# Optimization experiments

Measured on AMD Instinct MI355X. Metric: run time of the kernel, lower is better.

The kernel has to match this reference:

```python
import jax, jax.numpy as jnp
import numpy as np

B, S, D = 2, 1024, 1024
E, DG, L, H = 8, 256, 3, 2048
THR = 0.3


def setup_inputs() -> dict:
    key = jax.random.key(0)
    ks = jax.random.split(key, 10)
    hidden_states = jax.random.normal(ks[0], (B, S, D), jnp.float32)
    X = jax.random.normal(ks[1], (E, D), jnp.float32) * 0.02          # gate expert embeddings
    W_mlp = jax.random.normal(ks[2], (D, DG), jnp.float32) * (D ** -0.5)
    W_struct = jax.random.normal(ks[3], (D, DG), jnp.float32) * (D ** -0.5)
    conv_W = jax.random.normal(ks[4], (L, DG, DG), jnp.float32) * (DG ** -0.5)
    w_proj = jax.random.normal(ks[5], (DG,), jnp.float32) * (DG ** -0.5)
    W1 = jax.random.normal(ks[6], (E, D, H), jnp.float32) * (D ** -0.5)  # per-expert FFN up
    W2 = jax.random.normal(ks[7], (E, H, D), jnp.float32) * (H ** -0.5)  # per-expert FFN down
    lamb = jnp.asarray(1.5, jnp.float32)
    theta = jnp.asarray([E / 2.0], jnp.float32)
    count = jnp.zeros((E,), jnp.float32)
    # --- structural graph, precomputed once as in GoEgate.get_edges ---
    expn = np.asarray(jax.nn.silu(X @ W_struct))
    expn = expn / np.linalg.norm(expn, axis=1, keepdims=True)
    sim = expn @ expn.T
    y, perc, mask = 1.0, 0.0, None
    while perc < THR:
        mask = np.abs(sim) >= y
        perc = mask.sum() / (E * E)
        y -= 0.01
    N = E + 1  # experts + 1 token node per block
    A = np.zeros((N, N), np.float32)
    A[:E, :E] = mask
    A[:E, E] = 1.0
    A[E, :E] = 1.0
    A = A + np.eye(N, dtype=np.float32)  # GCNConv adds self-loops (experts end at 2, token node at 1)
    dinv = 1.0 / np.sqrt(A.sum(1))
    A_hat = jnp.asarray(dinv[:, None] * A * dinv[None, :])  # D^-1/2 (A+I) D^-1/2, [N, N]
    return dict(hidden_states=hidden_states, X=X, W_mlp=W_mlp, W_struct=W_struct,
                conv_W=conv_W, w_proj=w_proj, W1=W1, W2=W2, lamb=lamb, theta=theta,
                count=count, A_hat=A_hat, top_k=2)


def reference(hidden_states, X, W_mlp, W_struct, conv_W, w_proj, W1, W2,
              lamb, theta, count, A_hat, top_k):
    act = jax.nn.silu
    b, s, d = hidden_states.shape
    x2d = hidden_states.reshape(-1, d)            # [T, D]
    T = x2d.shape[0]
    # ---- GoEgate ----
    xg = act(x2d @ W_mlp)                          # [T, DG]
    expg = act(X @ W_struct)                       # [E, DG]
    node_x = jnp.concatenate(
        [jnp.broadcast_to(expg[None], (T, E, DG)), xg[:, None, :]], axis=1)  # [T, N, DG]
    for l in range(conv_W.shape[0]):
        node_x = act(jnp.einsum('nm,tmg->tng', A_hat, node_x @ conv_W[l]))   # GCN layer
    logits = (node_x @ w_proj)[:, :E]              # drop token-node column -> [T, E]
    probs = jax.nn.softmax(logits, axis=-1)        # router_logits after softmax
    rw, sel = jax.lax.top_k(probs, top_k)          # [T, k]
    # count accumulation (uses un-normalized topk weights)
    cmat = jnp.zeros((T, E), probs.dtype).at[jnp.arange(T)[:, None], sel].add(rw)
    now_count = count + cmat.sum(0) * top_k        # [E]
    rw = rw / rw.sum(-1, keepdims=True)            # normalize routing weights
    w_full = jnp.zeros((T, E), probs.dtype).at[jnp.arange(T)[:, None], sel].add(rw)
    # ---- per-expert FFN dispatch/combine (dense reference) ----
    h = act(jnp.einsum('td,edh->eth', x2d, W1))    # [E, T, H]
    expert_out = jnp.einsum('eth,ehd->etd', h, W2) # [E, T, D]
    final = jnp.einsum('etd,te->td', expert_out, w_full).reshape(b, s, d)
    loss_component = jnp.concatenate(
        [probs, now_count[None, :], jnp.broadcast_to(lamb, (1, E)),
         jnp.broadcast_to(theta, (1, E))], axis=0)  # [T+3, E]
    return final, loss_component
```

## Files before the change

### kernel.cpp

```cpp
#include <hip/hip_runtime.h>
#include <math.h>

#define TT 2048
#define Dm 1024
#define DGc 256
#define Ec 8
#define Nc 9
#define Hc 2048
#define PADMAX 5120
#define NT64MAX 80

typedef __attribute__((ext_vector_type(8))) short short8v;
typedef __attribute__((ext_vector_type(4))) float f32x4;

typedef __attribute__((address_space(1))) const void gvoid;
typedef __attribute__((address_space(3))) void svoid;

__device__ __forceinline__ void gll16(const void* g, void* l) {
    __builtin_amdgcn_global_load_lds((gvoid*)g, (svoid*)l, 16, 0, 0);
}

__device__ __forceinline__ float silu_f(float x) { return x / (1.f + __expf(-x)); }

__device__ __forceinline__ unsigned short bf16_rne(float f) {
    union { float f; unsigned u; } u; u.f = f;
    return (unsigned short)((u.u + 0x7fffu + ((u.u >> 16) & 1u)) >> 16);
}
__device__ __forceinline__ float bf16_to_f(unsigned short h) {
    union { unsigned u; float f; } u; u.u = ((unsigned)h) << 16; return u.f;
}
__device__ __forceinline__ void split2(float x, unsigned short& h, unsigned short& l) {
    h = bf16_rne(x);
    l = bf16_rne(x - bf16_to_f(h));
}

__device__ __forceinline__ void tsplit_body(const float* S, unsigned short* dh,
        unsigned short* dl, int R, int C, int r0, int c0, int tid, float (*t)[36]) {
    int i = tid >> 3, j4 = (tid & 7) * 4;
    *(float4*)&t[i][j4] = *(const float4*)&S[(size_t)(r0 + i) * C + c0 + j4];
    __syncthreads();
    int ci = tid >> 3, r4 = (tid & 7) * 4;
    ushort4 h, l;
    split2(t[r4 + 0][ci], h.x, l.x);
    split2(t[r4 + 1][ci], h.y, l.y);
    split2(t[r4 + 2][ci], h.z, l.z);
    split2(t[r4 + 3][ci], h.w, l.w);
    size_t o = (size_t)(c0 + ci) * R + r0 + r4;
    *(ushort4*)&dh[o] = h;
    *(ushort4*)&dl[o] = l;
}

__device__ __forceinline__ void tc64_body(const float* S, unsigned short* D,
        int R, int C, int r0, int c0, int tid, float* sb) {
    int r = tid >> 2;
    int cb = (tid & 3) * 16;
    const float* src = &S[(size_t)(r0 + r) * C + c0 + cb];
    int rot = 4 * (r & 15);
#pragma unroll
    for (int q = 0; q < 4; q++) {
        float4 v = *(const float4*)&src[q * 4];
        int cc = (cb + q * 4 + rot) & 63;
        *(float4*)&sb[r * 68 + cc] = v;
    }
    __syncthreads();
    int ci = tid >> 2;
    int rseg = (tid & 3) * 16;
    short8v o0, o1;
#pragma unroll
    for (int k = 0; k < 8; k++) {
        int r2 = rseg + k;
        int cc = (ci + 4 * (r2 & 15)) & 63;
        o0[k] = (short)bf16_rne(sb[r2 * 68 + cc]);
    }
#pragma unroll
    for (int k = 8; k < 16; k++) {
        int r2 = rseg + k;
        int cc = (ci + 4 * (r2 & 15)) & 63;
        o1[k - 8] = (short)bf16_rne(sb[r2 * 68 + cc]);
    }
    unsigned short* dst = &D[(size_t)(c0 + ci) * R + r0 + rseg];
    *(short8v*)&dst[0] = o0;
    *(short8v*)&dst[8] = o1;
}

__global__ __launch_bounds__(256) void k_tcslab(const float* src, unsigned short* dst,
                                                int R, int C) {
    __shared__ float sb[64 * 68];
    int per = (R / 64) * (C / 64);
    int e = blockIdx.x / per;
    int rem = blockIdx.x % per;
    int cpr = C / 64;
    int r0 = (rem / cpr) * 64;
    int c0 = (rem % cpr) * 64;
    tc64_body(src + (size_t)e * R * C, dst + (size_t)e * R * C, R, C, r0, c0,
              threadIdx.x, sb);
}

__global__ __launch_bounds__(256) void k_prep(const float* hs, const float* Wmlp,
        const float* convW, const float* X, const float* Wst,
        const float* count, const float* lamb, const float* theta,
        unsigned short* hs_hi, unsigned short* hs_lo,
        unsigned short* WmT_h, unsigned short* WmT_l,
        unsigned short* WcT_h, unsigned short* WcT_l,
        float* Xpart, float* out, int* tcnt,
        const float* W1, const float* W2,
        unsigned short* W1T, unsigned short* W2T) {
    __shared__ float sbuf[64 * 68];
    int b = blockIdx.x;
    int tid = threadIdx.x;
    if (b < 1024) {
        size_t i = ((size_t)b * 256 + tid) * 8;
        float4 v0 = *(const float4*)&hs[i];
        float4 v1 = *(const float4*)&hs[i + 4];
        ushort4 h0, l0, h1, l1;
        split2(v0.x, h0.x, l0.x); split2(v0.y, h0.y, l0.y);
        split2(v0.z, h0.z, l0.z); split2(v0.w, h0.w, l0.w);
        split2(v1.x, h1.x, l1.x); split2(v1.y, h1.y, l1.y);
        split2(v1.z, h1.z, l1.z); split2(v1.w, h1.w, l1.w);
        *(ushort4*)&hs_hi[i] = h0; *(ushort4*)&hs_hi[i + 4] = h1;
        *(ushort4*)&hs_lo[i] = l0; *(ushort4*)&hs_lo[i + 4] = l1;
    } else if (b < 1280) {
        int i2 = b - 1024;
        tsplit_body(Wmlp, WmT_h, WmT_l, Dm, DGc, (i2 >> 3) * 32, (i2 & 7) * 32,
                    tid, (float(*)[36])sbuf);
    } else if (b < 1472) {
        int i2 = b - 1280;
        int e = i2 >> 6, rem = i2 & 63;
        tsplit_body(convW + (size_t)e * DGc * DGc, WcT_h + (size_t)e * DGc * DGc,
                    WcT_l + (size_t)e * DGc * DGc, DGc, DGc,
                    (rem >> 3) * 32, (rem & 7) * 32, tid, (float(*)[36])sbuf);
    } else if (b < 1488) {
        float (*xs)[64] = (float(*)[64])sbuf;
        int p = b - 1472;
        int kb = p * 64;
        if (tid < 128) {
            int e = tid >> 4, k4 = (tid & 15) * 4;
            *(float4*)&xs[e][k4] = *(const float4*)&X[(size_t)e * Dm + kb + k4];
        }
        __syncthreads();
        float acc[Ec];
#pragma unroll
        for (int e = 0; e < Ec; e++) acc[e] = 0.f;
#pragma unroll 4
        for (int k = 0; k < 64; k++) {
            float w = Wst[(size_t)(kb + k) * DGc + tid];
#pragma unroll
            for (int e = 0; e < Ec; e++) acc[e] += xs[e][k] * w;
        }
#pragma unroll
        for (int e = 0; e < Ec; e++) Xpart[(size_t)p * Ec * DGc + e * DGc + tid] = acc[e];
    } else if (b == 1488) {
        if (tid < Ec) {
            float* loss = out + (size_t)TT * Dm;
            loss[(size_t)(TT + 1) * Ec + tid] = lamb[0];
            loss[(size_t)(TT + 2) * Ec + tid] = theta[0];
        }
        for (int i = tid; i < TT; i += 256) tcnt[i] = 0;
    } else {
        int i = b - 1489;
        if (i < 4096) {
            int e = i >> 9, rem = i & 511;
            int r0 = (rem >> 5) * 64, c0 = (rem & 31) * 64;
            tc64_body(W1 + (size_t)e * Dm * Hc, W1T + (size_t)e * Dm * Hc,
                      Dm, Hc, r0, c0, tid, sbuf);
        } else {
            i -= 4096;
            int e = i >> 9, rem = i & 511;
            int r0 = (rem >> 4) * 64, c0 = (rem & 15) * 64;
            tc64_body(W2 + (size_t)e * Hc * Dm, W2T + (size_t)e * Hc * Dm,
                      Hc, Dm, r0, c0, tid, sbuf);
        }
    }
}

__global__ __launch_bounds__(256) void k_gA(const float* Xpart, const float* W0,
                                            float* Gpart) {
    int g = threadIdx.x;
    int kb = blockIdx.x * 32;
    __shared__ float xs[Ec][32];
    {
        int m = g >> 5, k = g & 31;
        float s = 0.f;
#pragma unroll
        for (int p = 0; p < 16; p++)
            s += Xpart[(size_t)p * Ec * DGc + m * DGc + kb + k];
        xs[m][k] = silu_f(s);
    }
    __syncthreads();
    float acc[Ec];
#pragma unroll
    for (int e = 0; e < Ec; e++) acc[e] = 0.f;
#pragma unroll 4
    for (int k = 0; k < 32; k++) {
        float w = W0[(size_t)(kb + k) * DGc + g];
#pragma unroll
        for (int e = 0; e < Ec; e++) acc[e] += xs[e][k] * w;
    }
#pragma unroll
    for (int e = 0; e < Ec; e++)
        Gpart[(size_t)blockIdx.x * Ec * DGc + e * DGc + g] = acc[e];
}

__global__ __launch_bounds__(256) void k_s1fin(const float* Gpart, const float* Ahat,
                                               float* S1) {
    int g = threadIdx.x;
    float Gl[Ec];
#pragma unroll
    for (int m = 0; m < Ec; m++) {
        float s = 0.f;
#pragma unroll
        for (int kb = 0; kb < 8; kb++)
            s += Gpart[(size_t)kb * Ec * DGc + m * DGc + g];
        Gl[m] = s;
    }
#pragma unroll
    for (int n = 0; n < Nc; n++) {
        float s = 0.f;
#pragma unroll
        for (int m = 0; m < Ec; m++) s += Ahat[n * Nc + m] * Gl[m];
        S1[n * DGc + g] = s;
    }
}

template<int BM, int KD, int KS, int BK, int EPI>
__global__ __launch_bounds__(256) void gemm4s(const unsigned short* Ah,
        const unsigned short* Al, const unsigned short* Bh, const unsigned short* Bl,
        float* Cf, unsigned short* Oh, unsigned short* Ol) {
    constexpr int FM = BM / 32;
    constexpr int KLEN = KD / KS;
    constexpr int CH = BK / 8;
    constexpr int RPP = 256 / CH;
    constexpr int APASS = BM / RPP;
    constexpr int BPASS = 128 / RPP;
    constexpr int KKS = BK / 32;
    int m0 = blockIdx.x * BM, n0 = blockIdx.y * 128;
    int k0 = blockIdx.z * KLEN;
    __shared__ __align__(16) unsigned short AsH[BM * BK];
    __shared__ __align__(16) unsigned short AsL[BM * BK];
    __shared__ __align__(16) unsigned short BsH[128 * BK];
    __shared__ __align__(16) unsigned short BsL[128 * BK];
    int tid = threadIdx.x, lane = tid & 63, wid = tid >> 6;
    int wr = wid >> 1, wc = wid & 1, lo = lane & 15, hi = lane >> 4;

    f32x4 acc[FM][4];
#pragma unroll
    for (int m = 0; m < FM; m++)
#pragma unroll
        for (int n = 0; n < 4; n++) acc[m][n] = (f32x4)(0.f);

    int arow = tid / CH;
    int cswz = ((tid & (CH - 1)) ^ (arow & (CH - 1))) * 8;
    const unsigned short* AgH = Ah + (size_t)(m0 + arow) * KD + cswz;
    const unsigned short* AgL = Al + (size_t)(m0 + arow) * KD + cswz;
    const unsigned short* BgH = Bh + (size_t)(n0 + arow) * KD + cswz;
    const unsigned short* BgL = Bl + (size_t)(n0 + arow) * KD + cswz;

    for (int kb = k0; kb < k0 + KLEN; kb += BK) {
#pragma unroll
        for (int r = 0; r < APASS; r++) {
            gll16(AgH + (size_t)r * RPP * KD + kb, (char*)AsH + r * 4096 + tid * 16);
            gll16(AgL + (size_t)r * RPP * KD + kb, (char*)AsL + r * 4096 + tid * 16);
        }
#pragma unroll
        for (int r = 0; r < BPASS; r++) {
            gll16(BgH + (size_t)r * RPP * KD + kb, (char*)BsH + r * 4096 + tid * 16);
            gll16(BgL + (size_t)r * RPP * KD + kb, (char*)BsL + r * 4096 + tid * 16);
        }
        __syncthreads();
#pragma unroll
        for (int kk = 0; kk < KKS; kk++) {
            int csel = ((kk * 4 + hi) ^ (lo & (CH - 1))) * 8;
            short8v ah[FM], al[FM], bh[4], bl[4];
#pragma unroll
            for (int m = 0; m < FM; m++) {
                ah[m] = *(const short8v*)&AsH[(wr * (BM / 2) + m * 16 + lo) * BK + csel];
                al[m] = *(const short8v*)&AsL[(wr * (BM / 2) + m * 16 + lo) * BK + csel];
            }
#pragma unroll
            for (int n = 0; n < 4; n++) {
                bh[n] = *(const short8v*)&BsH[(wc * 64 + n * 16 + lo) * BK + csel];
                bl[n] = *(const short8v*)&BsL[(wc * 64 + n * 16 + lo) * BK + csel];
            }
#pragma unroll
            for (int m = 0; m < FM; m++)
#pragma unroll
                for (int n = 0; n < 4; n++)
                    acc[m][n] = __builtin_amdgcn_mfma_f32_16x16x32_bf16(ah[m], bh[n], acc[m][n], 0, 0, 0);
#pragma unroll
            for (int m = 0; m < FM; m++)
#pragma unroll
                for (int n = 0; n < 4; n++)
                    acc[m][n] = __builtin_amdgcn_mfma_f32_16x16x32_bf16(ah[m], bl[n], acc[m][n], 0, 0, 0);
#pragma unroll
            for (int m = 0; m < FM; m++)
#pragma unroll
                for (int n = 0; n < 4; n++)
                    acc[m][n] = __builtin_amdgcn_mfma_f32_16x16x32_bf16(al[m], bh[n], acc[m][n], 0, 0, 0);
        }
        __syncthreads();
    }

#pragma unroll
    for (int m = 0; m < FM; m++) {
#pragma unroll
        for (int n = 0; n < 4; n++) {
            int col = n0 + wc * 64 + n * 16 + lo;
#pragma unroll
            for (int r = 0; r < 4; r++) {
                int row = m0 + wr * (BM / 2) + m * 16 + hi * 4 + r;
                if (EPI == 0) {
                    Cf[(size_t)row * 256 + col] = acc[m][n][r];
                } else if (EPI == 3) {
                    Cf[((size_t)blockIdx.z * TT + row) * 256 + col] = acc[m][n][r];
                } else {
                    float s = silu_f(acc[m][n][r]);
                    unsigned short h, l;
                    split2(s, h, l);
                    Oh[(size_t)row * 256 + col] = h;
                    Ol[(size_t)row * 256 + col] = l;
                }
            }
        }
    }
}

__global__ __launch_bounds__(256) void k_finsplit(const float* src,
        unsigned short* dh, unsigned short* dl) {
    size_t i = ((size_t)blockIdx.x * 256 + threadIdx.x) * 4;
    float4 v0 = *(const float4*)&src[i];
    float4 v1 = *(const float4*)&src[(size_t)TT * DGc + i];
    float4 v2 = *(const float4*)&src[(size_t)2 * TT * DGc + i];
    float4 v3 = *(const float4*)&src[(size_t)3 * TT * DGc + i];
    float4 v = make_float4(v0.x + v1.x + v2.x + v3.x, v0.y + v1.y + v2.y + v3.y,
                           v0.z + v1.z + v2.z + v3.z, v0.w + v1.w + v2.w + v3.w);
    ushort4 h, l;
    split2(silu_f(v.x), h.x, l.x);
    split2(silu_f(v.y), h.y, l.y);
    split2(silu_f(v.z), h.z, l.z);
    split2(silu_f(v.w), h.w, l.w);
    *(ushort4*)&dh[i] = h;
    *(ushort4*)&dl[i] = l;
}

__global__ __launch_bounds__(256) void k_l1(const float* ypart, const float* S1,
        const float* Ahat, unsigned short* nh, unsigned short* nl) {
    int t = blockIdx.x, g = threadIdx.x;
    float yv = ypart[(size_t)t * DGc + g] + ypart[(size_t)TT * DGc + (size_t)t * DGc + g];
#pragma unroll
    for (int n = 0; n < Nc; n++) {
        float c = Ahat[n * Nc + Ec];
        float s = silu_f(S1[n * DGc + g] + c * yv);
        unsigned short h, l;
        split2(s, h, l);
        size_t o = ((size_t)t * Nc + n) * DGc + g;
        nh[o] = h; nl[o] = l;
    }
}

__global__ __launch_bounds__(256) void k_mix2(const float* Z, const float* Ahat,
        unsigned short* nh, unsigned short* nl) {
    int t = blockIdx.x, g = threadIdx.x;
    __shared__ float A[Nc * Nc];
    if (g < Nc * Nc) A[g] = Ahat[g];
    __syncthreads();
    float z[Nc];
#pragma unroll
    for (int m = 0; m < Nc; m++) z[m] = Z[((size_t)t * Nc + m) * DGc + g];
#pragma unroll
    for (int n = 0; n < Nc; n++) {
        float s = 0.f;
#pragma unroll
        for (int m = 0; m < Nc; m++) s += A[n * Nc + m] * z[m];
        s = silu_f(s);
        unsigned short h, l;
        split2(s, h, l);
        size_t o = ((size_t)t * Nc + n) * DGc + g;
        nh[o] = h; nl[o] = l;
    }
}

__global__ __launch_bounds__(256) void k_mix3(const float* Z, const float* Ahat,
        const float* wproj, float* out, int* sel, float* selv) {
    __shared__ float A[Nc * Nc];
    __shared__ float wp[DGc];
    int tid = threadIdx.x;
    if (tid < Nc * Nc) A[tid] = Ahat[tid];
    wp[tid] = wproj[tid];
    __syncthreads();
    int wid = tid >> 6, lane = tid & 63;
    int t = blockIdx.x * 4 + wid;
    float lg[Ec];
#pragma unroll
    for (int e = 0; e < Ec; e++) lg[e] = 0.f;
#pragma unroll
    for (int j = 0; j < 4; j++) {
        int g = j * 64 + lane;
        float z[Nc];
#pragma unroll
        for (int m = 0; m < Nc; m++) z[m] = Z[((size_t)t * Nc + m) * DGc + g];
#pragma unroll
        for (int e = 0; e < Ec; e++) {
            float s = 0.f;
#pragma unroll
            for (int m = 0; m < Nc; m++) s += A[e * Nc + m] * z[m];
            lg[e] += silu_f(s) * wp[g];
        }
    }
#pragma unroll
    for (int off = 32; off >= 1; off >>= 1) {
#pragma unroll
        for (int e = 0; e < Ec; e++) lg[e] += __shfl_xor(lg[e], off);
    }
    if (lane == 0) {
        float mx = -1e30f;
#pragma unroll
        for (int e = 0; e < Ec; e++) mx = fmaxf(mx, lg[e]);
        float pr[Ec], s = 0.f;
#pragma unroll
        for (int e = 0; e < Ec; e++) { pr[e] = __expf(lg[e] - mx); s += pr[e]; }
        float inv = 1.f / s;
        float* lrow = out + (size_t)TT * Dm + (size_t)t * Ec;
#pragma unroll
        for (int e = 0; e < Ec; e++) { pr[e] *= inv; lrow[e] = pr[e]; }
        int i0 = 0; float v0 = pr[0];
#pragma unroll
        for (int e = 1; e < Ec; e++) if (pr[e] > v0) { v0 = pr[e]; i0 = e; }
        int i1 = -1; float v1 = -1e30f;
#pragma unroll
        for (int e = 0; e < Ec; e++) if (e != i0 && pr[e] > v1) { v1 = pr[e]; i1 = e; }
        sel[t * 2] = i0; sel[t * 2 + 1] = i1;
        selv[t * 2] = v0; selv[t * 2 + 1] = v1;
    }
}

__global__ __launch_bounds__(256) void k_route(const int* sel, const float* selv,
        const float* count, float* out, int* cnt, int* toklist, float* wlist) {
    int e = blockIdx.x;
    int tid = threadIdx.x;
    int lane = tid & 63, wid = tid >> 6;
    __shared__ int wsum[4];
    __shared__ float wsumf[4];
    __shared__ int sbase;
    __shared__ float swtot;
    if (tid == 0) { sbase = 0; swtot = 0.f; }
    __syncthreads();
    for (int c = 0; c < TT; c += 256) {
        int t = c + tid;
        int i0 = sel[t * 2], i1 = sel[t * 2 + 1];
        float v0 = selv[t * 2], v1 = selv[t * 2 + 1];
        int f = 0; float vraw = 0.f;
        if (i0 == e) { f = 1; vraw = v0; }
        else if (i1 == e) { f = 1; vraw = v1; }
        float winv = 1.f / (v0 + v1);
        int ps = f;
        float pw = 2.f * vraw;
#pragma unroll
        for (int off = 1; off < 64; off <<= 1) {
            int s_ = __shfl_up(ps, off);
            float w_ = __shfl_up(pw, off);
            if (lane >= off) { ps += s_; pw += w_; }
        }
        if (lane == 63) { wsum[wid] = ps; wsumf[wid] = pw; }
        __syncthreads();
        int wpre = 0; float wpref = 0.f;
        for (int q = 0; q < wid; q++) { wpre += wsum[q]; wpref += wsumf[q]; }
        if (f) {
            int pos = sbase + wpre + ps - 1;
            toklist[e * TT + pos] = t;
            wlist[e * TT + pos] = vraw * winv;
        }
        __syncthreads();
        if (tid == 255) { sbase += wpre + ps; swtot += wpref + pw; }
        __syncthreads();
    }
    if (tid == 0) {
        cnt[e] = sbase;
        out[(size_t)TT * Dm + (size_t)TT * Ec + e] = count[e] + swtot;
    }
}

__global__ __launch_bounds__(256) void k_gather(const unsigned short* hs_hi,
        const int* cnt, const int* toklist, const float* wlist,
        unsigned short* xb, int* tcnt, int* tok2slot, float* tok2w) {
    int tid = threadIdx.x;
    int s = blockIdx.x * 2 + (tid >> 7);
    int j = (tid & 127) * 8;
    int e = -1, pos = 0, pad = 0, ce = 0;
#pragma unroll
    for (int q = 0; q < Ec; q++) {
        int cq = cnt[q];
        int span = ((cq + 63) >> 6) * 64;
        if (e < 0 && s < pad + span) { e = q; pos = s - pad; ce = cq; }
        pad += span;
    }
    int tok = -1; float w = 0.f;
    if (e >= 0 && pos < ce) { tok = toklist[e * TT + pos]; w = wlist[e * TT + pos]; }
    if (j == 0 && tok >= 0) {
        int idx = atomicAdd(&tcnt[tok], 1);
        tok2slot[tok * 2 + idx] = s;
        tok2w[tok * 2 + idx] = w;
    }
    short8v o;
    if (tok >= 0) {
        o = *(const short8v*)&hs_hi[(size_t)tok * Dm + j];
    } else {
        o = (short8v)(short)0;
    }
    *(short8v*)&xb[(size_t)s * Dm + j] = o;
}

template<int KDIM, int NDIM, int MODE, int KS>
__global__ __launch_bounds__(256) void k_mfma(const unsigned short* Abuf,
        const unsigned short* Wt, const int* cnt, unsigned short* outp) {
    constexpr int NY = NDIM / 128;
    constexpr int KLEN = KDIM / KS;
    constexpr int CPX = (NT64MAX * NY * KS) / 8;
    int bid = blockIdx.x;
    int flat = (bid & 7) * CPX + (bid >> 3);
    int tx = flat / (NY * KS);
    int rem = flat % (NY * KS);
    int y = rem / KS, ks = rem % KS;
    int e = -1, m0 = 0, acc_t = 0, pad = 0;
#pragma unroll
    for (int q = 0; q < Ec; q++) {
        int te = (cnt[q] + 63) >> 6;
        if (e < 0 && tx < acc_t + te) { e = q; m0 = pad + (tx - acc_t) * 64; }
        acc_t += te; pad += te * 64;
    }
    if (e < 0) return;
    int n0 = y * 128;
    int k0 = ks * KLEN;
    __shared__ __align__(16) unsigned short As[64 * 64];
    __shared__ __align__(16) unsigned short Bs[128 * 64];
    int tid = threadIdx.x;
    int lane = tid & 63;
    int wid = tid >> 6;
    int wr = wid >> 1, wc = wid & 1;
    int lo = lane & 15, hi = lane >> 4;

    f32x4 acc[2][4];
#pragma unroll
    for (int m = 0; m < 2; m++)
#pragma unroll
        for (int n = 0; n < 4; n++) acc[m][n] = (f32x4)(0.f);

    int arow = tid >> 3;
    int cswz = ((tid & 7) ^ (arow & 7)) * 8;
    const unsigned short* Ag = Abuf + (size_t)(m0 + arow) * KDIM + k0 + cswz;
    const unsigned short* Bg = Wt + (size_t)e * NDIM * KDIM
                               + (size_t)(n0 + arow) * KDIM + k0 + cswz;

    for (int kb = 0; kb < KLEN; kb += 64) {
        gll16(Ag + kb,                          (char*)As + tid * 16);
        gll16(Ag + 32 * (size_t)KDIM + kb,      (char*)As + 4096 + tid * 16);
        gll16(Bg + kb,                          (char*)Bs + tid * 16);
        gll16(Bg + 32 * (size_t)KDIM + kb,      (char*)Bs + 4096 + tid * 16);
        gll16(Bg + 64 * (size_t)KDIM + kb,      (char*)Bs + 8192 + tid * 16);
        gll16(Bg + 96 * (size_t)KDIM + kb,      (char*)Bs + 12288 + tid * 16);
        __syncthreads();
#pragma unroll
        for (int kk = 0; kk < 2; kk++) {
            int csel = ((kk * 4 + hi) ^ (lo & 7)) * 8;
            short8v a[2], b[4];
#pragma unroll
            for (int m = 0; m < 2; m++)
                a[m] = *(const short8v*)&As[(wr * 32 + m * 16 + lo) * 64 + csel];
#pragma unroll
            for (int n = 0; n < 4; n++)
                b[n] = *(const short8v*)&Bs[(wc * 64 + n * 16 + lo) * 64 + csel];
#pragma unroll
            for (int m = 0; m < 2; m++)
#pragma unroll
                for (int n = 0; n < 4; n++)
                    acc[m][n] = __builtin_amdgcn_mfma_f32_16x16x32_bf16(a[m], b[n], acc[m][n], 0, 0, 0);
        }
        __syncthreads();
    }

#pragma unroll
    for (int m = 0; m < 2; m++) {
#pragma unroll
        for (int n = 0; n < 4; n++) {
            int col = n0 + wc * 64 + n * 16 + lo;
#pragma unroll
            for (int r = 0; r < 4; r++) {
                int row = m0 + wr * 32 + m * 16 + hi * 4 + r;
                if (MODE == 0) {
                    outp[(size_t)row * NDIM + col] = bf16_rne(silu_f(acc[m][n][r]));
                } else {
                    outp[((size_t)ks * PADMAX + row) * Dm + col] = bf16_rne(acc[m][n][r]);
                }
            }
        }
    }
}

__global__ __launch_bounds__(256) void k_combine(const unsigned short* Opart,
        const int* tok2slot, const float* tok2w, float* out) {
    int t = blockIdx.x, tid = threadIdx.x;
    int s0 = tok2slot[t * 2], s1 = tok2slot[t * 2 + 1];
    float w0 = tok2w[t * 2], w1 = tok2w[t * 2 + 1];
    int c = tid * 4;
    ushort4 a0 = *(const ushort4*)&Opart[(size_t)s0 * Dm + c];
    ushort4 a1 = *(const ushort4*)&Opart[((size_t)PADMAX + s0) * Dm + c];
    ushort4 b0 = *(const ushort4*)&Opart[(size_t)s1 * Dm + c];
    ushort4 b1 = *(const ushort4*)&Opart[((size_t)PADMAX + s1) * Dm + c];
    float4 r;
    r.x = w0 * (bf16_to_f(a0.x) + bf16_to_f(a1.x)) + w1 * (bf16_to_f(b0.x) + bf16_to_f(b1.x));
    r.y = w0 * (bf16_to_f(a0.y) + bf16_to_f(a1.y)) + w1 * (bf16_to_f(b0.y) + bf16_to_f(b1.y));
    r.z = w0 * (bf16_to_f(a0.z) + bf16_to_f(a1.z)) + w1 * (bf16_to_f(b0.z) + bf16_to_f(b1.z));
    r.w = w0 * (bf16_to_f(a0.w) + bf16_to_f(a1.w)) + w1 * (bf16_to_f(b0.w) + bf16_to_f(b1.w));
    *(float4*)&out[(size_t)t * Dm + c] = r;
}

extern "C" void kernel_launch(void* const* d_in, const int* in_sizes, int n_in,
                              void* d_out, int out_size, void* d_ws, size_t ws_size,
                              hipStream_t stream) {
    const float* hs    = (const float*)d_in[0];
    const float* X     = (const float*)d_in[1];
    const float* Wmlp  = (const float*)d_in[2];
    const float* Wst   = (const float*)d_in[3];
    const float* convW = (const float*)d_in[4];
    const float* wproj = (const float*)d_in[5];
    const float* W1    = (const float*)d_in[6];
    const float* W2    = (const float*)d_in[7];
    const float* lamb  = (const float*)d_in[8];
    const float* theta = (const float*)d_in[9];
    const float* count = (const float*)d_in[10];
    const float* Ahat  = (const float*)d_in[11];
    float* out = (float*)d_out;
    char* ws = (char*)d_ws;

    int*            cnt     = (int*)(ws + 8192);
    float*          S1      = (float*)(ws + 9728);
    int*            toklist = (int*)(ws + 20480);
    float*          wlist   = (float*)(ws + 86016);
    int*            tcnt    = (int*)(ws + 151552);
    int*            tok2slot= (int*)(ws + 159744);
    float*          tok2w   = (float*)(ws + 176128);
    int*            sel     = (int*)(ws + 192512);
    float*          selv    = (float*)(ws + 208896);
    unsigned short* xb      = (unsigned short*)(ws + 237568);
    unsigned short* W1T     = (unsigned short*)(ws + 10723328);
    unsigned short* W2T     = (unsigned short*)(ws + 44277760);
    unsigned short* hb      = (unsigned short*)(ws + 77832192);
    unsigned short* Opart   = W1T;

    bool big = ws_size >= (size_t)174063616;
    char* G = big ? (ws + 98803712) : (ws + 10723328);
    unsigned short* hs_hi = (unsigned short*)(G);
    unsigned short* hs_lo = (unsigned short*)(G + 4194304);
    unsigned short* WmT_h = (unsigned short*)(G + 8388608);
    unsigned short* WmT_l = (unsigned short*)(G + 8912896);
    unsigned short* WcT_h = (unsigned short*)(G + 9437184);
    unsigned short* WcT_l = (unsigned short*)(G + 9830400);
    unsigned short* xg_h  = (unsigned short*)(G + 10223616);
    unsigned short* xg_l  = (unsigned short*)(G + 11272192);
    float*          ypart = (float*)(G + 12320768);
    unsigned short* n_h   = (unsigned short*)(G + 16515072);
    unsigned short* n_l   = (unsigned short*)(G + 25952256);
    float*          Zb    = (float*)(G + 35389440);
    float*          Gpart = (float*)(G + 54263808);
    float*          xgp   = (float*)(G + 54329344);
    float*          Xpart = (float*)(G + 62717952);

    int prep_blocks = big ? (1489 + 8192) : 1489;
    k_prep<<<prep_blocks, 256, 0, stream>>>(hs, Wmlp, convW, X, Wst, count, lamb,
                                            theta, hs_hi, hs_lo, WmT_h, WmT_l,
                                            WcT_h, WcT_l, Xpart, out, tcnt,
                                            W1, W2, W1T, W2T);
    k_gA<<<DGc / 32, 256, 0, stream>>>(Xpart, convW, Gpart);
    k_s1fin<<<1, 256, 0, stream>>>(Gpart, Ahat, S1);
    gemm4s<64, Dm, 4, 128, 3><<<dim3(TT / 64, 2, 4), 256, 0, stream>>>(
        hs_hi, hs_lo, WmT_h, WmT_l, xgp, nullptr, nullptr);
    k_finsplit<<<TT * DGc / 1024, 256, 0, stream>>>(xgp, xg_h, xg_l);
    gemm4s<64, DGc, 2, 128, 3><<<dim3(TT / 64, 2, 2), 256, 0, stream>>>(
        xg_h, xg_l, WcT_h, WcT_l, ypart, nullptr, nullptr);
    k_l1<<<TT, 256, 0, stream>>>(ypart, S1, Ahat, n_h, n_l);
    gemm4s<64, DGc, 1, 64, 0><<<dim3(TT * Nc / 64, 2, 1), 256, 0, stream>>>(
        n_h, n_l, WcT_h + 65536, WcT_l + 65536, Zb, nullptr, nullptr);
    k_mix2<<<TT, 256, 0, stream>>>(Zb, Ahat, n_h, n_l);
    gemm4s<64, DGc, 1, 64, 0><<<dim3(TT * Nc / 64, 2, 1), 256, 0, stream>>>(
        n_h, n_l, WcT_h + 131072, WcT_l + 131072, Zb, nullptr, nullptr);
    k_mix3<<<TT / 4, 256, 0, stream>>>(Zb, Ahat, wproj, out, sel, selv);
    k_route<<<Ec, 256, 0, stream>>>(sel, selv, count, out, cnt, toklist, wlist);
    k_gather<<<PADMAX / 2, 256, 0, stream>>>(hs_hi, cnt, toklist, wlist,
                                             xb, tcnt, tok2slot, tok2w);
    if (!big) {
        k_tcslab<<<Ec * (Dm / 64) * (Hc / 64), 256, 0, stream>>>(W1, W1T, Dm, Hc);
        k_tcslab<<<Ec * (Hc / 64) * (Dm / 64), 256, 0, stream>>>(W2, W2T, Hc, Dm);
    }
    k_mfma<Dm, Hc, 0, 1><<<NT64MAX * (Hc / 128), 256, 0, stream>>>(
        xb, W1T, cnt, hb);
    k_mfma<Hc, Dm, 1, 2><<<NT64MAX * (Dm / 128) * 2, 256, 0, stream>>>(
        hb, W2T, cnt, Opart);
    k_combine<<<TT, 256, 0, stream>>>(Opart, tok2slot, tok2w, out);
}
```

Before: 193.7 us.

## Spread expert weight transposes across gating GEMM launches to overlap with small GEMMs

Moves the W1/W2 fp32-to-bf16 transpose blocks out of the prep kernel and appends them as extra blocks to the three gating GEMM launches (2048 + 3072 + 3072). They now run alongside the small, under-filled GEMMs instead of serialising ahead of them. The GEMM grid is flattened to 1D, the K tile for the first two GEMMs drops from 128 to 64, and shared memory becomes one union buffer. The transpose LDS rotation also gets an extra row-group offset to reduce bank conflicts. The risk is that the heavy transpose blocks delay the critical-path GEMMs, or raise their LDS use and lower occupancy.

```diff
diff --git a/kernel.cpp b/kernel.cpp
--- a/kernel.cpp
+++ b/kernel.cpp
@@ -55,7 +55,7 @@
     int r = tid >> 2;
     int cb = (tid & 3) * 16;
     const float* src = &S[(size_t)(r0 + r) * C + c0 + cb];
-    int rot = 4 * (r & 15);
+    int rot = 4 * (r & 15) + 8 * (r >> 4);
 #pragma unroll
     for (int q = 0; q < 4; q++) {
         float4 v = *(const float4*)&src[q * 4];
@@ -69,13 +69,13 @@
 #pragma unroll
     for (int k = 0; k < 8; k++) {
         int r2 = rseg + k;
-        int cc = (ci + 4 * (r2 & 15)) & 63;
+        int cc = (ci + 4 * (r2 & 15) + 8 * (r2 >> 4)) & 63;
         o0[k] = (short)bf16_rne(sb[r2 * 68 + cc]);
     }
 #pragma unroll
     for (int k = 8; k < 16; k++) {
         int r2 = rseg + k;
-        int cc = (ci + 4 * (r2 & 15)) & 63;
+        int cc = (ci + 4 * (r2 & 15) + 8 * (r2 >> 4)) & 63;
         o1[k - 8] = (short)bf16_rne(sb[r2 * 68 + cc]);
     }
     unsigned short* dst = &D[(size_t)(c0 + ci) * R + r0 + rseg];
@@ -83,17 +83,26 @@
     *(short8v*)&dst[8] = o1;
 }
 
-__global__ __launch_bounds__(256) void k_tcslab(const float* src, unsigned short* dst,
-                                                int R, int C) {
+__device__ __forceinline__ void tc_dispatch(int i, const float* W1, const float* W2,
+        unsigned short* W1T, unsigned short* W2T, int tid, float* sb) {
+    if (i < 4096) {
+        int e = i >> 9, rem = i & 511;
+        int r0 = (rem >> 5) * 64, c0 = (rem & 31) * 64;
+        tc64_body(W1 + (size_t)e * Dm * Hc, W1T + (size_t)e * Dm * Hc,
+                  Dm, Hc, r0, c0, tid, sb);
+    } else {
+        i -= 4096;
+        int e = i >> 9, rem = i & 511;
+        int r0 = (rem >> 4) * 64, c0 = (rem & 15) * 64;
+        tc64_body(W2 + (size_t)e * Hc * Dm, W2T + (size_t)e * Hc * Dm,
+                  Hc, Dm, r0, c0, tid, sb);
+    }
+}
+
+__global__ __launch_bounds__(256) void k_tcslab(const float* W1, const float* W2,
+        unsigned short* W1T, unsigned short* W2T) {
     __shared__ float sb[64 * 68];
-    int per = (R / 64) * (C / 64);
-    int e = blockIdx.x / per;
-    int rem = blockIdx.x % per;
-    int cpr = C / 64;
-    int r0 = (rem / cpr) * 64;
-    int c0 = (rem % cpr) * 64;
-    tc64_body(src + (size_t)e * R * C, dst + (size_t)e * R * C, R, C, r0, c0,
-              threadIdx.x, sb);
+    tc_dispatch(blockIdx.x, W1, W2, W1T, W2T, threadIdx.x, sb);
 }
 
 __global__ __launch_bounds__(256) void k_prep(const float* hs, const float* Wmlp,
@@ -102,10 +111,8 @@
         unsigned short* hs_hi, unsigned short* hs_lo,
         unsigned short* WmT_h, unsigned short* WmT_l,
         unsigned short* WcT_h, unsigned short* WcT_l,
-        float* Xpart, float* out, int* tcnt,
-        const float* W1, const float* W2,
-        unsigned short* W1T, unsigned short* W2T) {
-    __shared__ float sbuf[64 * 68];
+        float* Xpart, float* out, int* tcnt) {
+    __shared__ float sbuf[32 * 36 > Ec * 64 ? 32 * 36 : Ec * 64];
     int b = blockIdx.x;
     int tid = threadIdx.x;
     if (b < 1024) {
@@ -149,27 +156,13 @@
         }
 #pragma unroll
         for (int e = 0; e < Ec; e++) Xpart[(size_t)p * Ec * DGc + e * DGc + tid] = acc[e];
-    } else if (b == 1488) {
+    } else {
         if (tid < Ec) {
             float* loss = out + (size_t)TT * Dm;
             loss[(size_t)(TT + 1) * Ec + tid] = lamb[0];
             loss[(size_t)(TT + 2) * Ec + tid] = theta[0];
         }
         for (int i = tid; i < TT; i += 256) tcnt[i] = 0;
-    } else {
-        int i = b - 1489;
-        if (i < 4096) {
-            int e = i >> 9, rem = i & 511;
-            int r0 = (rem >> 5) * 64, c0 = (rem & 31) * 64;
-            tc64_body(W1 + (size_t)e * Dm * Hc, W1T + (size_t)e * Dm * Hc,
-                      Dm, Hc, r0, c0, tid, sbuf);
-        } else {
-            i -= 4096;
-            int e = i >> 9, rem = i & 511;
-            int r0 = (rem >> 4) * 64, c0 = (rem & 15) * 64;
-            tc64_body(W2 + (size_t)e * Hc * Dm, W2T + (size_t)e * Hc * Dm,
-                      Hc, Dm, r0, c0, tid, sbuf);
-        }
     }
 }
 
@@ -222,10 +215,12 @@
     }
 }
 
-template<int BM, int KD, int KS, int BK, int EPI>
+template<int BM, int KD, int KS, int BK, int EPI, int NX>
 __global__ __launch_bounds__(256) void gemm4s(const unsigned short* Ah,
         const unsigned short* Al, const unsigned short* Bh, const unsigned short* Bl,
-        float* Cf, unsigned short* Oh, unsigned short* Ol) {
+        float* Cf, unsigned short* Oh, unsigned short* Ol,
+        const float* W1, const float* W2,
+        unsigned short* W1T, unsigned short* W2T, int tcBase) {
     constexpr int FM = BM / 32;
     constexpr int KLEN = KD / KS;
     constexpr int CH = BK / 8;
@@ -233,13 +228,24 @@
     constexpr int APASS = BM / RPP;
     constexpr int BPASS = 128 / RPP;
     constexpr int KKS = BK / 32;
-    int m0 = blockIdx.x * BM, n0 = blockIdx.y * 128;
-    int k0 = blockIdx.z * KLEN;
-    __shared__ __align__(16) unsigned short AsH[BM * BK];
-    __shared__ __align__(16) unsigned short AsL[BM * BK];
-    __shared__ __align__(16) unsigned short BsH[128 * BK];
-    __shared__ __align__(16) unsigned short BsL[128 * BK];
-    int tid = threadIdx.x, lane = tid & 63, wid = tid >> 6;
+    constexpr int NGEMM = NX * 2 * KS;
+    __shared__ __align__(16) unsigned char smem[(BM * BK + 128 * BK) * 4];
+    int tid = threadIdx.x;
+    int bid = blockIdx.x;
+    if (bid >= NGEMM) {
+        tc_dispatch(tcBase + (bid - NGEMM), W1, W2, W1T, W2T, tid, (float*)smem);
+        return;
+    }
+    unsigned short* AsH = (unsigned short*)smem;
+    unsigned short* AsL = AsH + BM * BK;
+    unsigned short* BsH = AsL + BM * BK;
+    unsigned short* BsL = BsH + 128 * BK;
+    int m0 = (bid % NX) * BM;
+    int rest = bid / NX;
+    int n0 = (rest & 1) * 128;
+    int kz = rest >> 1;
+    int k0 = kz * KLEN;
+    int lane = tid & 63, wid = tid >> 6;
     int wr = wid >> 1, wc = wid & 1, lo = lane & 15, hi = lane >> 4;
 
     f32x4 acc[FM][4];
@@ -311,7 +317,7 @@
                 if (EPI == 0) {
                     Cf[(size_t)row * 256 + col] = acc[m][n][r];
                 } else if (EPI == 3) {
-                    Cf[((size_t)blockIdx.z * TT + row) * 256 + col] = acc[m][n][r];
+                    Cf[((size_t)kz * TT + row) * 256 + col] = acc[m][n][r];
                 } else {
                     float s = silu_f(acc[m][n][r]);
                     unsigned short h, l;
@@ -664,31 +670,36 @@
     float*          xgp   = (float*)(G + 54329344);
     float*          Xpart = (float*)(G + 62717952);
 
-    int prep_blocks = big ? (1489 + 8192) : 1489;
-    k_prep<<<prep_blocks, 256, 0, stream>>>(hs, Wmlp, convW, X, Wst, count, lamb,
-                                            theta, hs_hi, hs_lo, WmT_h, WmT_l,
-                                            WcT_h, WcT_l, Xpart, out, tcnt,
-                                            W1, W2, W1T, W2T);
+    int tc_xg = big ? 2048 : 0;
+    int tc_l2 = big ? 3072 : 0;
+    int tc_l3 = big ? 3072 : 0;
+
+    k_prep<<<1489, 256, 0, stream>>>(hs, Wmlp, convW, X, Wst, count, lamb,
+                                     theta, hs_hi, hs_lo, WmT_h, WmT_l,
+                                     WcT_h, WcT_l, Xpart, out, tcnt);
     k_gA<<<DGc / 32, 256, 0, stream>>>(Xpart, convW, Gpart);
     k_s1fin<<<1, 256, 0, stream>>>(Gpart, Ahat, S1);
-    gemm4s<64, Dm, 4, 128, 3><<<dim3(TT / 64, 2, 4), 256, 0, stream>>>(
-        hs_hi, hs_lo, WmT_h, WmT_l, xgp, nullptr, nullptr);
+    gemm4s<64, Dm, 4, 64, 3, 32><<<256 + tc_xg, 256, 0, stream>>>(
+        hs_hi, hs_lo, WmT_h, WmT_l, xgp, nullptr, nullptr,
+        W1, W2, W1T, W2T, 0);
     k_finsplit<<<TT * DGc / 1024, 256, 0, stream>>>(xgp, xg_h, xg_l);
-    gemm4s<64, DGc, 2, 128, 3><<<dim3(TT / 64, 2, 2), 256, 0, stream>>>(
-        xg_h, xg_l, WcT_h, WcT_l, ypart, nullptr, nullptr);
+    gemm4s<64, DGc, 2, 64, 3, 32><<<128, 256, 0, stream>>>(
+        xg_h, xg_l, WcT_h, WcT_l, ypart, nullptr, nullptr,
+        W1, W2, W1T, W2T, 0);
     k_l1<<<TT, 256, 0, stream>>>(ypart, S1, Ahat, n_h, n_l);
-    gemm4s<64, DGc, 1, 64, 0><<<dim3(TT * Nc / 64, 2, 1), 256, 0, stream>>>(
-        n_h, n_l, WcT_h + 65536, WcT_l + 65536, Zb, nullptr, nullptr);
+    gemm4s<64, DGc, 1, 64, 0, 288><<<576 + tc_l2, 256, 0, stream>>>(
+        n_h, n_l, WcT_h + 65536, WcT_l + 65536, Zb, nullptr, nullptr,
+        W1, W2, W1T, W2T, 2048);
     k_mix2<<<TT, 256, 0, stream>>>(Zb, Ahat, n_h, n_l);
-    gemm4s<64, DGc, 1, 64, 0><<<dim3(TT * Nc / 64, 2, 1), 256, 0, stream>>>(
-        n_h, n_l, WcT_h + 131072, WcT_l + 131072, Zb, nullptr, nullptr);
+    gemm4s<64, DGc, 1, 64, 0, 288><<<576 + tc_l3, 256, 0, stream>>>(
+        n_h, n_l, WcT_h + 131072, WcT_l + 131072, Zb, nullptr, nullptr,
+        W1, W2, W1T, W2T, 5120);
     k_mix3<<<TT / 4, 256, 0, stream>>>(Zb, Ahat, wproj, out, sel, selv);
     k_route<<<Ec, 256, 0, stream>>>(sel, selv, count, out, cnt, toklist, wlist);
     k_gather<<<PADMAX / 2, 256, 0, stream>>>(hs_hi, cnt, toklist, wlist,
                                              xb, tcnt, tok2slot, tok2w);
     if (!big) {
-        k_tcslab<<<Ec * (Dm / 64) * (Hc / 64), 256, 0, stream>>>(W1, W1T, Dm, Hc);
-        k_tcslab<<<Ec * (Hc / 64) * (Dm / 64), 256, 0, stream>>>(W2, W2T, Hc, Dm);
+        k_tcslab<<<8192, 256, 0, stream>>>(W1, W2, W1T, W2T);
     }
     k_mfma<Dm, Hc, 0, 1><<<NT64MAX * (Hc / 128), 256, 0, stream>>>(
         xb, W1T, cnt, hb);
```

Result: slower. 198.3 us (+2.4%).
